# Performance work log

Measured on AMD Instinct MI355X. Metric: run time of the kernel, lower is better.

The kernel has to match this reference:

```python
import jax, jax.numpy as jnp
import numpy as np

VOCAB = 50000
D = 128      # word_embedding_size
H = 64       # attention_hidden_dim


def _doc_embed(words, emb_table, w_self, b_self):
    """words: (..., W) int -> (..., D) via tanh self-attention pooling over words."""
    we = emb_table[words]                                # (..., W, D)
    scores = jnp.tanh(we @ w_self + b_self)              # (..., W, 1)
    wgt = jax.nn.softmax(scores, axis=-2)                # softmax over word dim
    return jnp.sum(wgt * we, axis=-2)                    # (..., D)


def _attention(reviews_emb, query_emb, Wq, bq, w_red):
    """reviews_emb: (B,R,D), query_emb: (B,1,D) -> (B,D)."""
    B = query_emb.shape[0]
    pq = jnp.tanh(query_emb.reshape(B, D) @ Wq + bq)     # (B, D*H)
    pq = pq.reshape(B, D, H)
    s = jnp.einsum('brd,bdh->brh', reviews_emb, pq)      # (B,R,H)
    r = s @ w_red                                        # (B,R,1)
    w = jax.nn.softmax(r, axis=1)                        # softmax over reviews
    return jnp.sum(w * reviews_emb, axis=1)              # (B,D)


def setup_inputs() -> dict:
    key = jax.random.key(0)
    ks = jax.random.split(key, 9)
    B, R, W = 256, 20, 100
    user = jax.random.randint(ks[0], (B, R, W), 0, VOCAB)
    item = jax.random.randint(ks[1], (B, R, W), 0, VOCAB)
    query = jax.random.randint(ks[2], (B, W), 0, VOCAB)
    emb_table = jax.random.normal(ks[3], (VOCAB, D), dtype=jnp.float32) * 0.01
    w_self = jax.random.normal(ks[4], (D, 1), dtype=jnp.float32) * (1.0 / np.sqrt(D))
    b_self = jax.random.uniform(ks[5], (1,), dtype=jnp.float32, maxval=0.01)
    Wq = jax.random.normal(ks[6], (D, D * H), dtype=jnp.float32) * (1.0 / np.sqrt(D))
    bq = jax.random.uniform(ks[7], (D * H,), dtype=jnp.float32, maxval=0.01)
    w_red = jax.random.normal(ks[8], (H, 1), dtype=jnp.float32) * (1.0 / np.sqrt(H))
    pf = jnp.float32(0.5)  # personalized_factor
    return {"user_reviews_words": user, "item_reviews_words": item, "query": query,
            "emb_table": emb_table, "w_self": w_self, "b_self": b_self,
            "Wq": Wq, "bq": bq, "w_red": w_red, "pf": pf}


def reference(user_reviews_words, item_reviews_words, query,
              emb_table, w_self, b_self, Wq, bq, w_red, pf):
    # mode == 'test'
    user_emb = _doc_embed(user_reviews_words, emb_table, w_self, b_self)   # (B,R,D)
    item_emb = _doc_embed(item_reviews_words, emb_table, w_self, b_self)   # (B,R,D)
    q_emb = _doc_embed(query[:, None, :], emb_table, w_self, b_self)       # (B,1,D)
    user_entity = _attention(user_emb, q_emb, Wq, bq, w_red)               # (B,D)
    item_entity = _attention(item_emb, q_emb, Wq, bq, w_red)               # (B,D)
    personalized = user_entity + pf * q_emb[:, 0, :]
    return (personalized, item_entity)
```

## Files before the change

kernel.cpp:

```cpp
#include <hip/hip_runtime.h>
#include <math.h>

#define D 128
#define H 64
#define W 100
#define R 20
#define NB 256
#define NDOC_UI (NB * R)

__global__ __launch_bounds__(256) void doc_embed_kernel(
    const int* __restrict__ user_w, const int* __restrict__ item_w,
    const int* __restrict__ query_w,
    const float* __restrict__ emb, const float* __restrict__ w_self,
    const float* __restrict__ b_self,
    float* __restrict__ user_emb, float* __restrict__ item_emb,
    float* __restrict__ q_emb)
{
    __shared__ int   lds_words[W + 4];
    __shared__ float lds_esum[8];
    __shared__ __align__(16) float lds_part[8 * 128];

    int doc = blockIdx.x;
    const int* wp; float* outp;
    if (doc < NDOC_UI)          { wp = user_w  + doc * W;              outp = user_emb + doc * D; }
    else if (doc < 2*NDOC_UI)   { int t = doc - NDOC_UI;   wp = item_w  + t * W; outp = item_emb + t * D; }
    else                        { int t = doc - 2*NDOC_UI; wp = query_w + t * W; outp = q_emb    + t * D; }

    int tid    = threadIdx.x;
    int lane32 = tid & 31;
    int g      = tid >> 5;

    if (tid < W) lds_words[tid] = wp[tid];
    float4 ws4 = ((const float4*)w_self)[lane32];
    float  bs  = b_self[0];
    __syncthreads();

    float4 v[13];
    #pragma unroll
    for (int i = 0; i < 13; ++i) {
        int w = i * 8 + g;
        if (w < W)
            v[i] = ((const float4*)emb)[(size_t)lds_words[w] * 32 + lane32];
    }

    float4 acc = make_float4(0.f, 0.f, 0.f, 0.f);
    float  esum = 0.f;
    #pragma unroll
    for (int i = 0; i < 13; ++i) {
        int w = i * 8 + g;
        if (w < W) {
            float p = v[i].x * ws4.x + v[i].y * ws4.y + v[i].z * ws4.z + v[i].w * ws4.w;
            p += __shfl_xor(p, 16, 64);
            p += __shfl_xor(p, 8, 64);
            p += __shfl_xor(p, 4, 64);
            p += __shfl_xor(p, 2, 64);
            p += __shfl_xor(p, 1, 64);
            float e = expf(tanhf(p + bs));
            esum += e;
            acc.x += e * v[i].x;
            acc.y += e * v[i].y;
            acc.z += e * v[i].z;
            acc.w += e * v[i].w;
        }
    }
    *(float4*)&lds_part[g * 128 + lane32 * 4] = acc;
    if (lane32 == 0) lds_esum[g] = esum;
    __syncthreads();

    if (tid < 64) {
        float s = lds_esum[0] + lds_esum[1] + lds_esum[2] + lds_esum[3]
                + lds_esum[4] + lds_esum[5] + lds_esum[6] + lds_esum[7];
        float inv = 1.f / s;
        float2 o = make_float2(0.f, 0.f);
        #pragma unroll
        for (int gg = 0; gg < 8; ++gg) {
            float2 p2 = *(const float2*)&lds_part[gg * 128 + tid * 2];
            o.x += p2.x;
            o.y += p2.y;
        }
        o.x *= inv;
        o.y *= inv;
        ((float2*)outp)[tid] = o;
    }
}

__global__ __launch_bounds__(256) void pv_kernel(
    const float* __restrict__ q_emb, const float* __restrict__ Wq,
    const float* __restrict__ bq, const float* __restrict__ w_red,
    float* __restrict__ pv)
{
    __shared__ __align__(16) float qs[64 * 132];
    __shared__ __align__(16) float Wb[128 * 68];

    int dd  = blockIdx.x;
    int m0g = blockIdx.y * 64;
    int tid = threadIdx.x;

    {
        int rrow = tid >> 4;
        int f4   = tid & 15;
        #pragma unroll
        for (int pass = 0; pass < 4; ++pass) {
            int m = pass * 16 + rrow;
            float4 vq = ((const float4*)q_emb)[(m0g + m) * 32 + f4];
            *(float4*)&qs[m * 132 + f4 * 4] = vq;
        }
        #pragma unroll
        for (int pass = 0; pass < 8; ++pass) {
            int k = pass * 16 + rrow;
            float4 vw = ((const float4*)Wq)[k * 2048 + dd * 16 + f4];
            *(float4*)&Wb[k * 68 + f4 * 4] = vw;
        }
    }
    __syncthreads();

    int nthr = tid & 7;
    int mthr = tid >> 3;
    int n0 = nthr * 8;
    int m0 = mthr * 2;

    float acc[2][8];
    #pragma unroll
    for (int i = 0; i < 2; ++i)
        #pragma unroll
        for (int j = 0; j < 8; ++j) acc[i][j] = 0.f;

    for (int k = 0; k < 128; ++k) {
        float4 b0 = *(const float4*)&Wb[k * 68 + n0];
        float4 b1 = *(const float4*)&Wb[k * 68 + n0 + 4];
        float a0 = qs[(m0 + 0) * 132 + k];
        float a1 = qs[(m0 + 1) * 132 + k];
        float bv[8] = {b0.x, b0.y, b0.z, b0.w, b1.x, b1.y, b1.z, b1.w};
        #pragma unroll
        for (int j = 0; j < 8; ++j) {
            acc[0][j] += a0 * bv[j];
            acc[1][j] += a1 * bv[j];
        }
    }

    float4 bqa = ((const float4*)bq)[dd * 16 + nthr * 2];
    float4 bqb = ((const float4*)bq)[dd * 16 + nthr * 2 + 1];
    float4 wra = ((const float4*)w_red)[nthr * 2];
    float4 wrb = ((const float4*)w_red)[nthr * 2 + 1];
    float bqv[8] = {bqa.x, bqa.y, bqa.z, bqa.w, bqb.x, bqb.y, bqb.z, bqb.w};
    float wrv[8] = {wra.x, wra.y, wra.z, wra.w, wrb.x, wrb.y, wrb.z, wrb.w};

    #pragma unroll
    for (int i = 0; i < 2; ++i) {
        float s = 0.f;
        #pragma unroll
        for (int j = 0; j < 8; ++j)
            s += tanhf(acc[i][j] + bqv[j]) * wrv[j];
        s += __shfl_xor(s, 1, 64);
        s += __shfl_xor(s, 2, 64);
        s += __shfl_xor(s, 4, 64);
        if (nthr == 0) pv[(m0g + m0 + i) * 128 + dd] = s;
    }
}

__global__ __launch_bounds__(256) void attn_kernel(
    const float* __restrict__ user_emb, const float* __restrict__ item_emb,
    const float* __restrict__ q_emb, const float* __restrict__ pv,
    const float* __restrict__ pf, float* __restrict__ out)
{
    __shared__ float rev[R * 129];
    __shared__ float pvl[D];
    __shared__ float sc[R];

    int b   = blockIdx.x;
    int set = blockIdx.y;
    const float* revg = (set == 0 ? user_emb : item_emb) + b * R * D;
    int tid = threadIdx.x;

    for (int idx = tid; idx < R * D; idx += 256)
        rev[(idx >> 7) * 129 + (idx & 127)] = revg[idx];
    if (tid < D) pvl[tid] = pv[b * D + tid];
    __syncthreads();

    if (tid < R) {
        float s = 0.f;
        const float* row = &rev[tid * 129];
        #pragma unroll 16
        for (int k = 0; k < D; ++k) s += row[k] * pvl[k];
        sc[tid] = s;
    }
    __syncthreads();

    float m = -1e30f;
    for (int r = 0; r < R; ++r) m = fmaxf(m, sc[r]);
    float sum = 0.f;
    for (int r = 0; r < R; ++r) sum += expf(sc[r] - m);
    float inv = 1.f / sum;

    if (tid < D) {
        float acc = 0.f;
        for (int r = 0; r < R; ++r)
            acc += expf(sc[r] - m) * inv * rev[r * 129 + tid];
        if (set == 0) {
            acc += pf[0] * q_emb[b * D + tid];
            out[b * D + tid] = acc;
        } else {
            out[NB * D + b * D + tid] = acc;
        }
    }
}

extern "C" void kernel_launch(void* const* d_in, const int* in_sizes, int n_in,
                              void* d_out, int out_size, void* d_ws, size_t ws_size,
                              hipStream_t stream) {
    const int*   user_w  = (const int*)d_in[0];
    const int*   item_w  = (const int*)d_in[1];
    const int*   query_w = (const int*)d_in[2];
    const float* emb     = (const float*)d_in[3];
    const float* w_self  = (const float*)d_in[4];
    const float* b_self  = (const float*)d_in[5];
    const float* Wq      = (const float*)d_in[6];
    const float* bq      = (const float*)d_in[7];
    const float* w_red   = (const float*)d_in[8];
    const float* pf      = (const float*)d_in[9];

    float* ws       = (float*)d_ws;
    float* user_emb = ws;
    float* item_emb = user_emb + NDOC_UI * D;
    float* q_emb    = item_emb + NDOC_UI * D;
    float* pv       = q_emb    + NB * D;
    float* out      = (float*)d_out;

    doc_embed_kernel<<<2 * NDOC_UI + NB, 256, 0, stream>>>(
        user_w, item_w, query_w, emb, w_self, b_self, user_emb, item_emb, q_emb);
    pv_kernel<<<dim3(128, 4), 256, 0, stream>>>(q_emb, Wq, bq, w_red, pv);
    attn_kernel<<<dim3(NB, 2), 256, 0, stream>>>(user_emb, item_emb, q_emb, pv, pf, out);
}
```

Measured before the change: 168.1 us.

## Map one document per half-wave in doc embedding and use fast tanh/exp

The doc-embedding kernel now gives each 32-lane group its own document. Each group holds its word indices in registers and broadcasts them with ds_bpermute, which removes the LDS word staging, both block barriers and the cross-group reduction. Gathers are issued in batches of 10 words per group, and occupancy is hinted at 7 blocks per CU. The precise tanhf and expf calls are replaced with __expf plus a hardware-reciprocal tanh approximation, and the other kernels also move to __expf. This trades a little precision for cheaper transcendentals, and each group now loads fewer gathers at a time than the earlier 13-deep prefetch.

```diff
diff --git a/kernel.cpp b/kernel.cpp
--- a/kernel.cpp
+++ b/kernel.cpp
@@ -8,7 +8,15 @@
 #define NB 256
 #define NDOC_UI (NB * R)
 
-__global__ __launch_bounds__(256) void doc_embed_kernel(
+__device__ __forceinline__ float fast_tanh(float x) {
+    float u = __expf(2.0f * x);
+    return 1.0f - 2.0f * __builtin_amdgcn_rcpf(1.0f + u);
+}
+__device__ __forceinline__ float fast_exp_tanh(float x) {
+    return __expf(fast_tanh(x));
+}
+
+__global__ __launch_bounds__(256, 7) void doc_embed_kernel(
     const int* __restrict__ user_w, const int* __restrict__ item_w,
     const int* __restrict__ query_w,
     const float* __restrict__ emb, const float* __restrict__ w_self,
@@ -16,72 +24,66 @@
     float* __restrict__ user_emb, float* __restrict__ item_emb,
     float* __restrict__ q_emb)
 {
-    __shared__ int   lds_words[W + 4];
-    __shared__ float lds_esum[8];
-    __shared__ __align__(16) float lds_part[8 * 128];
-
-    int doc = blockIdx.x;
-    const int* wp; float* outp;
-    if (doc < NDOC_UI)          { wp = user_w  + doc * W;              outp = user_emb + doc * D; }
-    else if (doc < 2*NDOC_UI)   { int t = doc - NDOC_UI;   wp = item_w  + t * W; outp = item_emb + t * D; }
-    else                        { int t = doc - 2*NDOC_UI; wp = query_w + t * W; outp = q_emb    + t * D; }
-
     int tid    = threadIdx.x;
     int lane32 = tid & 31;
-    int g      = tid >> 5;
-
-    if (tid < W) lds_words[tid] = wp[tid];
+    int grp    = tid >> 5;
+    int doc    = blockIdx.x * 8 + grp;
+
+    const int* wp; float* outp;
+    if (doc < NDOC_UI)        { wp = user_w + doc * W;               outp = user_emb + doc * D; }
+    else if (doc < 2*NDOC_UI) { int t = doc - NDOC_UI;   wp = item_w  + t * W; outp = item_emb + t * D; }
+    else                      { int t = doc - 2*NDOC_UI; wp = query_w + t * W; outp = q_emb    + t * D; }
+
+    int wreg[4];
+    #pragma unroll
+    for (int k = 0; k < 4; ++k) {
+        int idx = k * 32 + lane32;
+        wreg[k] = wp[idx > W - 1 ? W - 1 : idx];
+    }
+
     float4 ws4 = ((const float4*)w_self)[lane32];
     float  bs  = b_self[0];
-    __syncthreads();
-
-    float4 v[13];
-    #pragma unroll
-    for (int i = 0; i < 13; ++i) {
-        int w = i * 8 + g;
-        if (w < W)
-            v[i] = ((const float4*)emb)[(size_t)lds_words[w] * 32 + lane32];
-    }
-
-    float4 acc = make_float4(0.f, 0.f, 0.f, 0.f);
+    const float4* emb4 = (const float4*)emb;
+
+    int permbase = (tid & 32) * 4;
+
+    float4 acc  = make_float4(0.f, 0.f, 0.f, 0.f);
     float  esum = 0.f;
-    #pragma unroll
-    for (int i = 0; i < 13; ++i) {
-        int w = i * 8 + g;
-        if (w < W) {
-            float p = v[i].x * ws4.x + v[i].y * ws4.y + v[i].z * ws4.z + v[i].w * ws4.w;
+
+    #pragma unroll
+    for (int c = 0; c < 10; ++c) {
+        int word[10];
+        #pragma unroll
+        for (int j = 0; j < 10; ++j) {
+            int w = c * 10 + j;
+            word[j] = __builtin_amdgcn_ds_bpermute(permbase | ((w & 31) * 4),
+                                                   wreg[w >> 5]);
+        }
+        float4 v[10];
+        #pragma unroll
+        for (int j = 0; j < 10; ++j)
+            v[j] = emb4[(size_t)word[j] * 32 + lane32];
+
+        #pragma unroll
+        for (int j = 0; j < 10; ++j) {
+            float p = v[j].x * ws4.x + v[j].y * ws4.y + v[j].z * ws4.z + v[j].w * ws4.w;
             p += __shfl_xor(p, 16, 64);
             p += __shfl_xor(p, 8, 64);
             p += __shfl_xor(p, 4, 64);
             p += __shfl_xor(p, 2, 64);
             p += __shfl_xor(p, 1, 64);
-            float e = expf(tanhf(p + bs));
+            float e = fast_exp_tanh(p + bs);
             esum += e;
-            acc.x += e * v[i].x;
-            acc.y += e * v[i].y;
-            acc.z += e * v[i].z;
-            acc.w += e * v[i].w;
-        }
-    }
-    *(float4*)&lds_part[g * 128 + lane32 * 4] = acc;
-    if (lane32 == 0) lds_esum[g] = esum;
-    __syncthreads();
-
-    if (tid < 64) {
-        float s = lds_esum[0] + lds_esum[1] + lds_esum[2] + lds_esum[3]
-                + lds_esum[4] + lds_esum[5] + lds_esum[6] + lds_esum[7];
-        float inv = 1.f / s;
-        float2 o = make_float2(0.f, 0.f);
-        #pragma unroll
-        for (int gg = 0; gg < 8; ++gg) {
-            float2 p2 = *(const float2*)&lds_part[gg * 128 + tid * 2];
-            o.x += p2.x;
-            o.y += p2.y;
-        }
-        o.x *= inv;
-        o.y *= inv;
-        ((float2*)outp)[tid] = o;
-    }
+            acc.x += e * v[j].x;
+            acc.y += e * v[j].y;
+            acc.z += e * v[j].z;
+            acc.w += e * v[j].w;
+        }
+    }
+
+    float inv = 1.0f / esum;
+    acc.x *= inv; acc.y *= inv; acc.z *= inv; acc.w *= inv;
+    ((float4*)outp)[lane32] = acc;
 }
 
 __global__ __launch_bounds__(256) void pv_kernel(
@@ -150,7 +152,7 @@
         float s = 0.f;
         #pragma unroll
         for (int j = 0; j < 8; ++j)
-            s += tanhf(acc[i][j] + bqv[j]) * wrv[j];
+            s += fast_tanh(acc[i][j] + bqv[j]) * wrv[j];
         s += __shfl_xor(s, 1, 64);
         s += __shfl_xor(s, 2, 64);
         s += __shfl_xor(s, 4, 64);
@@ -189,13 +191,13 @@
     float m = -1e30f;
     for (int r = 0; r < R; ++r) m = fmaxf(m, sc[r]);
     float sum = 0.f;
-    for (int r = 0; r < R; ++r) sum += expf(sc[r] - m);
+    for (int r = 0; r < R; ++r) sum += __expf(sc[r] - m);
     float inv = 1.f / sum;
 
     if (tid < D) {
         float acc = 0.f;
         for (int r = 0; r < R; ++r)
-            acc += expf(sc[r] - m) * inv * rev[r * 129 + tid];
+            acc += __expf(sc[r] - m) * inv * rev[r * 129 + tid];
         if (set == 0) {
             acc += pf[0] * q_emb[b * D + tid];
             out[b * D + tid] = acc;
@@ -226,7 +228,7 @@
     float* pv       = q_emb    + NB * D;
     float* out      = (float*)d_out;
 
-    doc_embed_kernel<<<2 * NDOC_UI + NB, 256, 0, stream>>>(
+    doc_embed_kernel<<<(2 * NDOC_UI + NB) / 8, 256, 0, stream>>>(
         user_w, item_w, query_w, emb, w_self, b_self, user_emb, item_emb, q_emb);
     pv_kernel<<<dim3(128, 4), 256, 0, stream>>>(q_emb, Wq, bq, w_red, pv);
     attn_kernel<<<dim3(NB, 2), 256, 0, stream>>>(user_emb, item_emb, q_emb, pv, pf, out);
```

New measurement: 175.4 us. 1.04x slower.
